# Kernel tuning notes

Hardware: AMD Instinct MI355X
Metric: run time of the kernel (lower is better)

The kernel has to match this reference:

```python
import jax, jax.numpy as jnp
import numpy as np

TEMPERATURE = 0.1
SINGLE_POS = False
EPS = 1e-8  # torch CosineSimilarity eps
B, D = 8192, 128
N_DATA = 100000


def setup_inputs() -> dict:
    key = jax.random.key(0)
    k1, k2, k3, k4 = jax.random.split(key, 4)
    features = jax.random.normal(k1, (B, D), dtype=jnp.float32)
    data_ix = jax.random.randint(k2, (B,), 0, N_DATA, dtype=jnp.int64)
    targets_t = jax.random.randint(k3, (N_DATA,), 0, 2, dtype=jnp.int64)
    targets_p = jax.random.randint(k4, (N_DATA,), 0, 2, dtype=jnp.int64)
    return {"features": features, "data_ix": data_ix,
            "targets_t": targets_t, "targets_p": targets_p}


def reference(features, data_ix, targets_t, targets_p):
    tt = targets_t[data_ix]  # [B]
    tp = targets_p[data_ix]  # [B]

    # cosine similarity matrix [B, B] (torch CosineSimilarity semantics)
    norms = jnp.linalg.norm(features, axis=1)  # [B]
    dots = features @ features.T               # [B, B]
    sim = dots / jnp.maximum(norms[:, None] * norms[None, :], EPS)
    logits = sim / TEMPERATURE                 # log(exp(sim/T)) == sim/T
    exp_sim = jnp.exp(logits)

    # pos: same true label, different predicted label; neg: reversed
    same_t = tt[:, None] == tt[None, :]
    same_p = tp[:, None] == tp[None, :]
    pos_mask = same_t & ~same_p   # excludes self automatically
    neg_mask = ~same_t & same_p

    pos_cnt = pos_mask.sum(axis=1)  # [B]
    neg_cnt = neg_mask.sum(axis=1)  # [B]

    exp_pos_sum = jnp.sum(jnp.where(pos_mask, exp_sim, 0.0), axis=1)  # [B]
    exp_neg_sum = jnp.sum(jnp.where(neg_mask, exp_sim, 0.0), axis=1)  # [B]

    if SINGLE_POS:
        # per-pair denominator: log(exp_neg_sum + exp_pos_ij)
        log_denom = jnp.log(exp_neg_sum[:, None] + exp_sim)  # [B, B]
        log_probs_sum = jnp.sum(jnp.where(pos_mask, logits - log_denom, 0.0), axis=1)
    else:
        log_denom = jnp.log(exp_neg_sum + exp_pos_sum)  # [B]
        log_probs_sum = jnp.sum(jnp.where(pos_mask, logits - log_denom[:, None], 0.0), axis=1)

    valid = (pos_cnt > 0) & (neg_cnt > 0)
    mean_log_probs = jnp.where(valid,
                               log_probs_sum / jnp.maximum(pos_cnt, 1).astype(logits.dtype),
                               0.0)
    loss = -jnp.sum(mean_log_probs) / features.shape[0]
    return loss
```

## Files before the change

kernel.cpp:

```cpp
#include <hip/hip_runtime.h>


#define NB 8192
#define ND 128
#define NIB 64
#define JS 16
#define NH 8
#define TEMP_INV 10.0f
#define LOG2E 1.4426950408889634f
#define EXPK (TEMP_INV * LOG2E)

typedef __attribute__((ext_vector_type(8))) short short8;
typedef __attribute__((ext_vector_type(4))) float f32x4;

#define OFF_G    0
#define OFF_CLS  (NB * ND * 2)
#define OFF_CNT  (OFF_CLS + NB)
#define OFF_EPP  (OFF_CNT + 128)
#define OFF_ENP  (OFF_EPP + NB * 4 * JS)
#define OFF_LSP  (OFF_ENP + NB * 4 * JS)
#define OFF_CO   OFF_EPP
#define OFF_RL   (OFF_EPP + NB)

__device__ __forceinline__ unsigned short f2bf(float x) {
    unsigned int u = __float_as_uint(x);
    unsigned int r = (u + 0x7FFFu + ((u >> 16) & 1u)) >> 16;
    return (unsigned short)r;
}

__device__ __forceinline__ float fast_exp2(float x) {
#if __has_builtin(__builtin_amdgcn_exp2f)
    return __builtin_amdgcn_exp2f(x);
#else
    return exp2f(x);
#endif
}

typedef const __attribute__((address_space(1))) void gas_void;
typedef __attribute__((address_space(3))) void las_void;
__device__ __forceinline__ void gload_lds16(const void* g, void* s) {
    __builtin_amdgcn_global_load_lds((gas_void*)g, (las_void*)s, 16, 0, 0);
}

__global__ __launch_bounds__(1024) void classify_kernel(
    const int* __restrict__ dix, const int* __restrict__ tt, const int* __restrict__ tp,
    unsigned char* __restrict__ clsO, unsigned short* __restrict__ rlocal,
    int* __restrict__ cntP, float* __restrict__ out)
{
    __shared__ int lh[4];
    const int h = blockIdx.x, tid = threadIdx.x;
    if (tid < 4) lh[tid] = 0;
    __syncthreads();
    const int row = h * 1024 + tid;
    const int ix  = dix[row];
    const int c   = ((tt[ix] & 1) << 1) | (tp[ix] & 1);
    clsO[row] = (unsigned char)c;
    rlocal[row] = (unsigned short)atomicAdd(&lh[c], 1);
    if (h == 0 && tid == 0) *out = 0.0f;
    __syncthreads();
    if (tid < 4) cntP[h * 4 + tid] = lh[tid];
}

__global__ __launch_bounds__(256) void normscatter_kernel(
    const float* __restrict__ F, const unsigned char* __restrict__ clsO,
    const unsigned short* __restrict__ rlocal, const int* __restrict__ cntP,
    unsigned short* __restrict__ G, unsigned char* __restrict__ clsS)
{
    const int row  = blockIdx.x * 4 + (threadIdx.x >> 6);
    const int lane = threadIdx.x & 63;
    const int c = clsO[row];
    const int h = row >> 10;
    int base = (int)rlocal[row];
    #pragma unroll
    for (int cc = 0; cc < 3; ++cc)
        if (cc < c) {
            #pragma unroll
            for (int hh = 0; hh < NH; ++hh) base += cntP[hh * 4 + cc];
        }
    #pragma unroll
    for (int hh = 0; hh < NH - 1; ++hh)
        if (hh < h) base += cntP[hh * 4 + c];

    const float2 v = *(const float2*)(F + row * ND + lane * 2);
    float ss = v.x * v.x + v.y * v.y;
    #pragma unroll
    for (int m = 1; m < 64; m <<= 1) ss += __shfl_xor(ss, m, 64);
    const float inv = rsqrtf(fmaxf(ss, 1e-24f));
    ushort2 st; st.x = f2bf(v.x * inv); st.y = f2bf(v.y * inv);
    *(ushort2*)(G + base * ND + lane * 2) = st;
    if (lane == 0) clsS[base] = (unsigned char)c;
}

__device__ __forceinline__ void stage_panel(
    const unsigned short* __restrict__ G, unsigned short* Blds,
    int rbase, int wu, int lrow4, int lpos)
{
    #pragma unroll
    for (int j = 0; j < 4; ++j) {
        const int pr = wu * 16 + j * 4 + lrow4;
        int rowG = rbase + pr;
        rowG = (rowG < NB - 1) ? rowG : (NB - 1);
        const int chunk = (lpos - pr) & 15;
        gload_lds16(G + rowG * ND + chunk * 8, Blds + (wu * 16 + j * 4) * ND);
    }
}

template<int MODE>
__device__ __forceinline__ void seg_panels(
    const unsigned short* __restrict__ G, unsigned short* Blds0,
    unsigned short* Blds1, const short8 (&A)[2][4],
    float (&Ep)[8], float (&En)[8], float (&Ls)[8],
    const float (&wp)[8], const float (&wn)[8],
    int cs, int ce, int p0, int p1, int wu, int lane)
{
    const int lrow4 = lane >> 4, lpos = lane & 15;
    const int q = lane >> 4, l16 = lane & 15;

    stage_panel(G, Blds0, cs + p0 * 64, wu, lrow4, lpos);
    __syncthreads();
    #pragma unroll 1
    for (int p = p0; p < p1; ++p) {
        const int cur = (p - p0) & 1;
        unsigned short* bufC = cur ? Blds1 : Blds0;
        if (p + 1 < p1)
            stage_panel(G, cur ? Blds0 : Blds1, cs + (p + 1) * 64, wu, lrow4, lpos);
        if (MODE != 0) {
            #pragma unroll
            for (int st = 0; st < 4; ++st) {
                const int j0 = cs + p * 64 + st * 16;
                if (j0 >= ce) break;
                short8 Bf[4];
                #pragma unroll
                for (int c = 0; c < 4; ++c) {
                    const int slot = (c * 4 + q + l16) & 15;
                    Bf[c] = *(const short8*)&bufC[(st * 16 + l16) * ND + slot * 8];
                }
                f32x4 acc0 = {0.f, 0.f, 0.f, 0.f}, acc1 = {0.f, 0.f, 0.f, 0.f};
                #pragma unroll
                for (int c = 0; c < 4; ++c)
                    acc0 = __builtin_amdgcn_mfma_f32_16x16x32_bf16(A[0][c], Bf[c], acc0, 0, 0, 0);
                #pragma unroll
                for (int c = 0; c < 4; ++c)
                    acc1 = __builtin_amdgcn_mfma_f32_16x16x32_bf16(A[1][c], Bf[c], acc1, 0, 0, 0);
                if (j0 + 16 <= ce) {
                    #pragma unroll
                    for (int r = 0; r < 4; ++r) {
                        const float sv0 = acc0[r], sv1 = acc1[r];
                        const float e0 = fast_exp2(sv0 * EXPK);
                        const float e1 = fast_exp2(sv1 * EXPK);
                        if (MODE == 1) {
                            Ep[r] += e0;      Ls[r] += sv0;
                            Ep[4 + r] += e1;  Ls[4 + r] += sv1;
                        } else if (MODE == 2) {
                            En[r] += e0;      En[4 + r] += e1;
                        } else {
                            Ep[r]     = fmaf(wp[r],     e0,  Ep[r]);
                            Ls[r]     = fmaf(wp[r],     sv0, Ls[r]);
                            Ep[4 + r] = fmaf(wp[4 + r], e1,  Ep[4 + r]);
                            Ls[4 + r] = fmaf(wp[4 + r], sv1, Ls[4 + r]);
                            En[r]     = fmaf(wn[r],     e0, En[r]);
                            En[4 + r] = fmaf(wn[4 + r], e1, En[4 + r]);
                        }
                    }
                } else {
                    const float vm = ((j0 + l16) < ce) ? 1.f : 0.f;
                    #pragma unroll
                    for (int r = 0; r < 4; ++r) {
                        const float sv0 = acc0[r] * vm, sv1 = acc1[r] * vm;
                        const float e0 = fast_exp2(sv0 * EXPK) * vm;
                        const float e1 = fast_exp2(sv1 * EXPK) * vm;
                        if (MODE == 1) {
                            Ep[r] += e0;      Ls[r] += sv0;
                            Ep[4 + r] += e1;  Ls[4 + r] += sv1;
                        } else if (MODE == 2) {
                            En[r] += e0;      En[4 + r] += e1;
                        } else {
                            Ep[r]     = fmaf(wp[r],     e0,  Ep[r]);
                            Ls[r]     = fmaf(wp[r],     sv0, Ls[r]);
                            Ep[4 + r] = fmaf(wp[4 + r], e1,  Ep[4 + r]);
                            Ls[4 + r] = fmaf(wp[4 + r], sv1, Ls[4 + r]);
                            En[r]     = fmaf(wn[r],     e0, En[r]);
                            En[4 + r] = fmaf(wn[4 + r], e1, En[4 + r]);
                        }
                    }
                }
            }
        }
        __syncthreads();
    }
}

__global__ __launch_bounds__(256) __attribute__((amdgpu_waves_per_eu(3, 4)))
void sim_kernel(
    const unsigned short* __restrict__ G, const unsigned char* __restrict__ clsS,
    const int* __restrict__ cntP,
    float* __restrict__ EpP, float* __restrict__ EnP, float* __restrict__ LsP)
{
    __shared__ unsigned short Blds[2][64 * 128];

    const int ib = blockIdx.x & (NIB - 1);
    const int jb = blockIdx.x >> 6;
    const int wave = threadIdx.x >> 6, lane = threadIdx.x & 63;
    const int q = lane >> 4, l16 = lane & 15;
    const int ri = ib * 128 + wave * 32;
    const int wu = __builtin_amdgcn_readfirstlane(wave);

    short8 A[2][4];
    #pragma unroll
    for (int t = 0; t < 2; ++t)
        #pragma unroll
        for (int c = 0; c < 4; ++c)
            A[t][c] = *(const short8*)(G + (ri + 16 * t + l16) * ND + c * 32 + q * 8);

    const unsigned int rcLo = *(const unsigned int*)(clsS + ri + 4 * q);
    const unsigned int rcHi = *(const unsigned int*)(clsS + ri + 16 + 4 * q);
    const int wF = clsS[ri], wL = clsS[ri + 31];
    const int bF = clsS[ib * 128], bL = clsS[ib * 128 + 127];

    float Ep[8], En[8], Ls[8];
    #pragma unroll
    for (int i = 0; i < 8; ++i) { Ep[i] = 0.f; En[i] = 0.f; Ls[i] = 0.f; }
    float wp[8], wn[8];

    int cs = 0;
    #pragma unroll 1
    for (int s = 0; s < 4; ++s) {
        int len = 0;
        #pragma unroll
        for (int h = 0; h < NH; ++h) len += cntP[h * 4 + s];
        const int ce = cs + len;
        const int s1 = s ^ 1, s2 = s ^ 2;
        const bool aPb = (s1 >= bF) && (s1 <= bL);
        const bool aNb = (s2 >= bF) && (s2 <= bL);
        if (aPb || aNb) {
            const int np = (len + 63) >> 6;
            const int p0 = (jb * np) >> 4;
            const int p1 = ((jb + 1) * np) >> 4;
            if (p0 < p1) {
                if (wF == wL) {
                    if (s1 == wF)
                        seg_panels<1>(G, Blds[0], Blds[1], A, Ep, En, Ls, wp, wn, cs, ce, p0, p1, wu, lane);
                    else if (s2 == wF)
                        seg_panels<2>(G, Blds[0], Blds[1], A, Ep, En, Ls, wp, wn, cs, ce, p0, p1, wu, lane);
                    else
                        seg_panels<0>(G, Blds[0], Blds[1], A, Ep, En, Ls, wp, wn, cs, ce, p0, p1, wu, lane);
                } else {
                    #pragma unroll
                    for (int r = 0; r < 4; ++r) {
                        const int cLo = (rcLo >> (8 * r)) & 0xff;
                        const int cHi = (rcHi >> (8 * r)) & 0xff;
                        wp[r]     = (cLo == s1) ? 1.f : 0.f;
                        wp[4 + r] = (cHi == s1) ? 1.f : 0.f;
                        wn[r]     = (cLo == s2) ? 1.f : 0.f;
                        wn[4 + r] = (cHi == s2) ? 1.f : 0.f;
                    }
                    seg_panels<3>(G, Blds[0], Blds[1], A, Ep, En, Ls, wp, wn, cs, ce, p0, p1, wu, lane);
                }
            }
        }
        cs = ce;
    }

    #pragma unroll
    for (int m = 1; m < 16; m <<= 1)
        #pragma unroll
        for (int i = 0; i < 8; ++i) {
            Ep[i] += __shfl_xor(Ep[i], m, 64);
            En[i] += __shfl_xor(En[i], m, 64);
            Ls[i] += __shfl_xor(Ls[i], m, 64);
        }
    if (l16 == 0) {
        #pragma unroll
        for (int t = 0; t < 2; ++t)
            #pragma unroll
            for (int r = 0; r < 4; ++r) {
                const int row = ri + 16 * t + 4 * q + r;
                const int i = t * 4 + r;
                EpP[jb * NB + row] = Ep[i];
                EnP[jb * NB + row] = En[i];
                LsP[jb * NB + row] = Ls[i];
            }
    }
}

__global__ __launch_bounds__(256) void finalize_kernel(
    const float* __restrict__ EpP, const float* __restrict__ EnP,
    const float* __restrict__ LsP, const unsigned char* __restrict__ clsS,
    const int* __restrict__ cntP, float* __restrict__ out)
{
    const int i = blockIdx.x * 256 + threadIdx.x;
    int tot[4] = {0, 0, 0, 0};
    #pragma unroll
    for (int hh = 0; hh < NH; ++hh)
        #pragma unroll
        for (int cc = 0; cc < 4; ++cc) tot[cc] += cntP[hh * 4 + cc];
    const int c = clsS[i];
    const int pc = c ^ 1, nc = c ^ 2;
    const int pcnt = (pc == 0) ? tot[0] : (pc == 1) ? tot[1] : (pc == 2) ? tot[2] : tot[3];
    const int ncnt = (nc == 0) ? tot[0] : (nc == 1) ? tot[1] : (nc == 2) ? tot[2] : tot[3];
    float ep = 0.f, en = 0.f, ls = 0.f;
    #pragma unroll
    for (int jb = 0; jb < JS; ++jb) {
        ep += EpP[jb * NB + i];
        en += EnP[jb * NB + i];
        ls += LsP[jb * NB + i];
    }
    float contrib = 0.0f;
    if (pcnt > 0 && ncnt > 0) {
        const float ld = logf(ep + en);
        contrib = -(TEMP_INV * ls - (float)pcnt * ld) / ((float)pcnt * (float)NB);
    }
    #pragma unroll
    for (int m = 1; m < 64; m <<= 1) contrib += __shfl_xor(contrib, m, 64);
    __shared__ float wsum[4];
    if ((threadIdx.x & 63) == 0) wsum[threadIdx.x >> 6] = contrib;
    __syncthreads();
    if (threadIdx.x == 0)
        atomicAdd(out, wsum[0] + wsum[1] + wsum[2] + wsum[3]);
}

extern "C" void kernel_launch(void* const* d_in, const int* in_sizes, int n_in,
                              void* d_out, int out_size, void* d_ws, size_t ws_size,
                              hipStream_t stream) {
    const float* F = (const float*)d_in[0];
    const int* dix = (const int*)d_in[1];
    const int* tt  = (const int*)d_in[2];
    const int* tp  = (const int*)d_in[3];
    float* out = (float*)d_out;

    char* ws = (char*)d_ws;
    unsigned short* G   = (unsigned short*)(ws + OFF_G);
    unsigned char* clsS = (unsigned char*)(ws + OFF_CLS);
    int* cntP           = (int*)(ws + OFF_CNT);
    float* EpP          = (float*)(ws + OFF_EPP);
    float* EnP          = (float*)(ws + OFF_ENP);
    float* LsP          = (float*)(ws + OFF_LSP);
    unsigned char* clsO = (unsigned char*)(ws + OFF_CO);
    unsigned short* rl  = (unsigned short*)(ws + OFF_RL);

    classify_kernel<<<NH, 1024, 0, stream>>>(dix, tt, tp, clsO, rl, cntP, out);
    normscatter_kernel<<<2048, 256, 0, stream>>>(F, clsO, rl, cntP, G, clsS);
    sim_kernel<<<NIB * JS, 256, 0, stream>>>(G, clsS, cntP, EpP, EnP, LsP);
    finalize_kernel<<<NB / 256, 256, 0, stream>>>(EpP, EnP, LsP, clsS, cntP, out);
}
```

Measured before the change: 102.4 us.

## Split sim kernel work across 8 waves with 16 rows each

Raises the sim kernel block from 4 to 8 waves, so each wave covers 16 rows of the 128-row block instead of 32. Each wave now holds one A fragment set and one accumulator tile, and the panel staging is split across 8 waves. The aim is lower register pressure and more waves for latency hiding. In exchange, each B fragment read from LDS feeds only one MFMA instead of two, which doubles LDS read traffic per FLOP, and the waves_per_eu hint is removed.

```diff
diff --git a/kernel.cpp b/kernel.cpp
--- a/kernel.cpp
+++ b/kernel.cpp
@@ -96,21 +96,21 @@
     int rbase, int wu, int lrow4, int lpos)
 {
     #pragma unroll
-    for (int j = 0; j < 4; ++j) {
-        const int pr = wu * 16 + j * 4 + lrow4;
+    for (int j = 0; j < 2; ++j) {
+        const int pr = wu * 8 + j * 4 + lrow4;
         int rowG = rbase + pr;
         rowG = (rowG < NB - 1) ? rowG : (NB - 1);
         const int chunk = (lpos - pr) & 15;
-        gload_lds16(G + rowG * ND + chunk * 8, Blds + (wu * 16 + j * 4) * ND);
+        gload_lds16(G + rowG * ND + chunk * 8, Blds + (wu * 8 + j * 4) * ND);
     }
 }
 
 template<int MODE>
 __device__ __forceinline__ void seg_panels(
     const unsigned short* __restrict__ G, unsigned short* Blds0,
-    unsigned short* Blds1, const short8 (&A)[2][4],
-    float (&Ep)[8], float (&En)[8], float (&Ls)[8],
-    const float (&wp)[8], const float (&wn)[8],
+    unsigned short* Blds1, const short8 (&A)[4],
+    float (&Ep)[4], float (&En)[4], float (&Ls)[4],
+    const float (&wp)[4], const float (&wn)[4],
     int cs, int ce, int p0, int p1, int wu, int lane)
 {
     const int lrow4 = lane >> 4, lpos = lane & 15;
@@ -135,52 +135,35 @@
                     const int slot = (c * 4 + q + l16) & 15;
                     Bf[c] = *(const short8*)&bufC[(st * 16 + l16) * ND + slot * 8];
                 }
-                f32x4 acc0 = {0.f, 0.f, 0.f, 0.f}, acc1 = {0.f, 0.f, 0.f, 0.f};
+                f32x4 acc = {0.f, 0.f, 0.f, 0.f};
                 #pragma unroll
                 for (int c = 0; c < 4; ++c)
-                    acc0 = __builtin_amdgcn_mfma_f32_16x16x32_bf16(A[0][c], Bf[c], acc0, 0, 0, 0);
-                #pragma unroll
-                for (int c = 0; c < 4; ++c)
-                    acc1 = __builtin_amdgcn_mfma_f32_16x16x32_bf16(A[1][c], Bf[c], acc1, 0, 0, 0);
+                    acc = __builtin_amdgcn_mfma_f32_16x16x32_bf16(A[c], Bf[c], acc, 0, 0, 0);
                 if (j0 + 16 <= ce) {
                     #pragma unroll
                     for (int r = 0; r < 4; ++r) {
-                        const float sv0 = acc0[r], sv1 = acc1[r];
-                        const float e0 = fast_exp2(sv0 * EXPK);
-                        const float e1 = fast_exp2(sv1 * EXPK);
-                        if (MODE == 1) {
-                            Ep[r] += e0;      Ls[r] += sv0;
-                            Ep[4 + r] += e1;  Ls[4 + r] += sv1;
-                        } else if (MODE == 2) {
-                            En[r] += e0;      En[4 + r] += e1;
-                        } else {
-                            Ep[r]     = fmaf(wp[r],     e0,  Ep[r]);
-                            Ls[r]     = fmaf(wp[r],     sv0, Ls[r]);
-                            Ep[4 + r] = fmaf(wp[4 + r], e1,  Ep[4 + r]);
-                            Ls[4 + r] = fmaf(wp[4 + r], sv1, Ls[4 + r]);
-                            En[r]     = fmaf(wn[r],     e0, En[r]);
-                            En[4 + r] = fmaf(wn[4 + r], e1, En[4 + r]);
+                        const float sv = acc[r];
+                        const float e  = fast_exp2(sv * EXPK);
+                        if (MODE == 1)      { Ep[r] += e; Ls[r] += sv; }
+                        else if (MODE == 2) { En[r] += e; }
+                        else {
+                            Ep[r] = fmaf(wp[r], e,  Ep[r]);
+                            Ls[r] = fmaf(wp[r], sv, Ls[r]);
+                            En[r] = fmaf(wn[r], e,  En[r]);
                         }
                     }
                 } else {
                     const float vm = ((j0 + l16) < ce) ? 1.f : 0.f;
                     #pragma unroll
                     for (int r = 0; r < 4; ++r) {
-                        const float sv0 = acc0[r] * vm, sv1 = acc1[r] * vm;
-                        const float e0 = fast_exp2(sv0 * EXPK) * vm;
-                        const float e1 = fast_exp2(sv1 * EXPK) * vm;
-                        if (MODE == 1) {
-                            Ep[r] += e0;      Ls[r] += sv0;
-                            Ep[4 + r] += e1;  Ls[4 + r] += sv1;
-                        } else if (MODE == 2) {
-                            En[r] += e0;      En[4 + r] += e1;
-                        } else {
-                            Ep[r]     = fmaf(wp[r],     e0,  Ep[r]);
-                            Ls[r]     = fmaf(wp[r],     sv0, Ls[r]);
-                            Ep[4 + r] = fmaf(wp[4 + r], e1,  Ep[4 + r]);
-                            Ls[4 + r] = fmaf(wp[4 + r], sv1, Ls[4 + r]);
-                            En[r]     = fmaf(wn[r],     e0, En[r]);
-                            En[4 + r] = fmaf(wn[4 + r], e1, En[4 + r]);
+                        const float sv = acc[r] * vm;
+                        const float e  = fast_exp2(sv * EXPK) * vm;
+                        if (MODE == 1)      { Ep[r] += e; Ls[r] += sv; }
+                        else if (MODE == 2) { En[r] += e; }
+                        else {
+                            Ep[r] = fmaf(wp[r], e,  Ep[r]);
+                            Ls[r] = fmaf(wp[r], sv, Ls[r]);
+                            En[r] = fmaf(wn[r], e,  En[r]);
                         }
                     }
                 }
@@ -190,8 +173,7 @@
     }
 }
 
-__global__ __launch_bounds__(256) __attribute__((amdgpu_waves_per_eu(3, 4)))
-void sim_kernel(
+__global__ __launch_bounds__(512) void sim_kernel(
     const unsigned short* __restrict__ G, const unsigned char* __restrict__ clsS,
     const int* __restrict__ cntP,
     float* __restrict__ EpP, float* __restrict__ EnP, float* __restrict__ LsP)
@@ -202,25 +184,22 @@
     const int jb = blockIdx.x >> 6;
     const int wave = threadIdx.x >> 6, lane = threadIdx.x & 63;
     const int q = lane >> 4, l16 = lane & 15;
-    const int ri = ib * 128 + wave * 32;
+    const int ri = ib * 128 + wave * 16;
     const int wu = __builtin_amdgcn_readfirstlane(wave);
 
-    short8 A[2][4];
-    #pragma unroll
-    for (int t = 0; t < 2; ++t)
-        #pragma unroll
-        for (int c = 0; c < 4; ++c)
-            A[t][c] = *(const short8*)(G + (ri + 16 * t + l16) * ND + c * 32 + q * 8);
-
-    const unsigned int rcLo = *(const unsigned int*)(clsS + ri + 4 * q);
-    const unsigned int rcHi = *(const unsigned int*)(clsS + ri + 16 + 4 * q);
-    const int wF = clsS[ri], wL = clsS[ri + 31];
+    short8 A[4];
+    #pragma unroll
+    for (int c = 0; c < 4; ++c)
+        A[c] = *(const short8*)(G + (ri + l16) * ND + c * 32 + q * 8);
+
+    const unsigned int rc = *(const unsigned int*)(clsS + ri + 4 * q);
+    const int wF = clsS[ri], wL = clsS[ri + 15];
     const int bF = clsS[ib * 128], bL = clsS[ib * 128 + 127];
 
-    float Ep[8], En[8], Ls[8];
-    #pragma unroll
-    for (int i = 0; i < 8; ++i) { Ep[i] = 0.f; En[i] = 0.f; Ls[i] = 0.f; }
-    float wp[8], wn[8];
+    float Ep[4], En[4], Ls[4];
+    #pragma unroll
+    for (int i = 0; i < 4; ++i) { Ep[i] = 0.f; En[i] = 0.f; Ls[i] = 0.f; }
+    float wp[4], wn[4];
 
     int cs = 0;
     #pragma unroll 1
@@ -247,12 +226,9 @@
                 } else {
                     #pragma unroll
                     for (int r = 0; r < 4; ++r) {
-                        const int cLo = (rcLo >> (8 * r)) & 0xff;
-                        const int cHi = (rcHi >> (8 * r)) & 0xff;
-                        wp[r]     = (cLo == s1) ? 1.f : 0.f;
-                        wp[4 + r] = (cHi == s1) ? 1.f : 0.f;
-                        wn[r]     = (cLo == s2) ? 1.f : 0.f;
-                        wn[4 + r] = (cHi == s2) ? 1.f : 0.f;
+                        const int cr = (rc >> (8 * r)) & 0xff;
+                        wp[r] = (cr == s1) ? 1.f : 0.f;
+                        wn[r] = (cr == s2) ? 1.f : 0.f;
                     }
                     seg_panels<3>(G, Blds[0], Blds[1], A, Ep, En, Ls, wp, wn, cs, ce, p0, p1, wu, lane);
                 }
@@ -264,22 +240,19 @@
     #pragma unroll
     for (int m = 1; m < 16; m <<= 1)
         #pragma unroll
-        for (int i = 0; i < 8; ++i) {
+        for (int i = 0; i < 4; ++i) {
             Ep[i] += __shfl_xor(Ep[i], m, 64);
             En[i] += __shfl_xor(En[i], m, 64);
             Ls[i] += __shfl_xor(Ls[i], m, 64);
         }
     if (l16 == 0) {
         #pragma unroll
-        for (int t = 0; t < 2; ++t)
-            #pragma unroll
-            for (int r = 0; r < 4; ++r) {
-                const int row = ri + 16 * t + 4 * q + r;
-                const int i = t * 4 + r;
-                EpP[jb * NB + row] = Ep[i];
-                EnP[jb * NB + row] = En[i];
-                LsP[jb * NB + row] = Ls[i];
-            }
+        for (int r = 0; r < 4; ++r) {
+            const int row = ri + 4 * q + r;
+            EpP[jb * NB + row] = Ep[r];
+            EnP[jb * NB + row] = En[r];
+            LsP[jb * NB + row] = Ls[r];
+        }
     }
 }
 
@@ -340,6 +313,6 @@
 
     classify_kernel<<<NH, 1024, 0, stream>>>(dix, tt, tp, clsO, rl, cntP, out);
     normscatter_kernel<<<2048, 256, 0, stream>>>(F, clsO, rl, cntP, G, clsS);
-    sim_kernel<<<NIB * JS, 256, 0, stream>>>(G, clsS, cntP, EpP, EnP, LsP);
+    sim_kernel<<<NIB * JS, 512, 0, stream>>>(G, clsS, cntP, EpP, EnP, LsP);
     finalize_kernel<<<NB / 256, 256, 0, stream>>>(EpP, EnP, LsP, clsS, cntP, out);
 }
```

Measured after the change: 101.9 us, median of 2. About the same (-0.4%).
